# Performance work log

Hardware: AMD Instinct MI355X
Metric: run time of the kernel (lower is better)

The kernel has to match this reference:

```python
import jax, jax.numpy as jnp
import numpy as np

N = 50000          # num nodes
E = 800000         # num edges
NEG_SLOPE = 0.2    # leaky relu slope for attention logits


def gat_layer(h, W, al, ar, src, dst, res_W=None, res_identity=False, apply_elu=False):
    """One GATConv layer (DGL semantics, dropout=0, fc bias-free).
    h: [N, F_in]; W: [F_in, H*D]; al, ar: [H, D]. Returns [N, H, D]."""
    H, D = al.shape
    feat = (h @ W).reshape(N, H, D)                      # projected features
    el = jnp.sum(feat * al, axis=-1)                     # [N, H]
    er = jnp.sum(feat * ar, axis=-1)                     # [N, H]
    e = jax.nn.leaky_relu(el[src] + er[dst], NEG_SLOPE)  # [E, H] edge logits
    # numerically-stable edge softmax segmented over destination nodes
    m = jax.ops.segment_max(e, dst, num_segments=N)      # [N, H]
    m = jnp.where(jnp.isfinite(m), m, 0.0)               # nodes with no in-edges
    ex = jnp.exp(e - m[dst])
    den = jax.ops.segment_sum(ex, dst, num_segments=N)   # [N, H]
    alpha = ex / (den[dst] + 1e-9)                       # [E, H]
    # message passing: gather src feats, weight by alpha, scatter-add to dst
    out = jax.ops.segment_sum(feat[src] * alpha[..., None], dst, num_segments=N)
    if res_identity:
        out = out + h.reshape(N, H, D)
    elif res_W is not None:
        out = out + (h @ res_W).reshape(N, H, D)
    if apply_elu:
        out = jax.nn.elu(out)
    return out


def setup_inputs() -> dict:
    key = jax.random.key(0)
    ks = jax.random.split(key, 14)
    s = 0.1  # keep attention logits tame
    return {
        "features": jax.random.normal(ks[0], (N, 128), jnp.float32),
        "W0": jax.random.normal(ks[1], (128, 128), jnp.float32) * s,
        "al0": jax.random.normal(ks[2], (4, 32), jnp.float32) * s,
        "ar0": jax.random.normal(ks[3], (4, 32), jnp.float32) * s,
        "W1": jax.random.normal(ks[4], (128, 128), jnp.float32) * s,
        "al1": jax.random.normal(ks[5], (4, 32), jnp.float32) * s,
        "ar1": jax.random.normal(ks[6], (4, 32), jnp.float32) * s,
        "W2": jax.random.normal(ks[7], (128, 40), jnp.float32) * s,
        "al2": jax.random.normal(ks[8], (1, 40), jnp.float32) * s,
        "ar2": jax.random.normal(ks[9], (1, 40), jnp.float32) * s,
        "resW2": jax.random.normal(ks[10], (128, 40), jnp.float32) * s,
        "src": jax.random.randint(ks[11], (E,), 0, N, jnp.int32),
        "dst": jax.random.randint(ks[12], (E,), 0, N, jnp.int32),
    }


def reference(features, W0, al0, ar0, W1, al1, ar1, W2, al2, ar2, resW2, src, dst):
    # hidden layer 0: no residual, elu, flatten heads
    h = gat_layer(features, W0, al0, ar0, src, dst, apply_elu=True).reshape(N, -1)
    # hidden layer 1: residual (identity since in == heads*out), elu, flatten
    h = gat_layer(h, W1, al1, ar1, src, dst, res_identity=True, apply_elu=True).reshape(N, -1)
    # output layer: residual projection, no activation, mean over heads
    logits = gat_layer(h, W2, al2, ar2, src, dst, res_W=resW2).mean(axis=1)
    return logits
```

## Files before the change

kernel.cpp:

```cpp
#include <hip/hip_runtime.h>
#include <hip/hip_fp16.h>

#define NNODES 50000
#define NEDGES 800000
#define NBUCK 196
#define NCHUNK 256
#define CHUNK 3125

typedef _Float16 f16x8 __attribute__((ext_vector_type(8)));
typedef float f32x4 __attribute__((ext_vector_type(4)));


__global__ __launch_bounds__(256) void k_packhist(const int* __restrict__ src,
                                                  const int* __restrict__ dst,
                                                  unsigned* __restrict__ pack,
                                                  int* __restrict__ hist) {
  __shared__ int h[NBUCK];
  int t = threadIdx.x, c = blockIdx.x;
  for (int i = t; i < NBUCK; i += 256) h[i] = 0;
  __syncthreads();
  int beg = c * CHUNK;
  for (int q = t; q < CHUNK; q += 256) {
    int e = beg + q;
    unsigned d = (unsigned)dst[e], sv = (unsigned)src[e];
    pack[e] = (d << 16) | sv;
    atomicAdd(&h[d >> 8], 1);
  }
  __syncthreads();
  for (int i = t; i < NBUCK; i += 256) hist[i * NCHUNK + c] = h[i];
}

__global__ __launch_bounds__(1024) void k_scanall(const int* __restrict__ hist,
                                                  int* __restrict__ off) {
  __shared__ int sb[1024];
  int t = threadIdx.x;
  const int P = (NBUCK * NCHUNK) / 1024;
  int base = t * P;
  int s = 0;
  for (int i = 0; i < P; ++i) s += hist[base + i];
  sb[t] = s;
  __syncthreads();
  for (int o = 1; o < 1024; o <<= 1) {
    int x = (t >= o) ? sb[t - o] : 0;
    __syncthreads();
    sb[t] += x;
    __syncthreads();
  }
  int ex = sb[t] - s;
  for (int i = 0; i < P; ++i) {
    int v = hist[base + i];
    off[base + i] = ex;
    ex += v;
  }
}

__global__ __launch_bounds__(256) void k_partition(const unsigned* __restrict__ pack,
                                                   const int* __restrict__ off,
                                                   unsigned* __restrict__ bucketed) {
  __shared__ int cur[NBUCK];
  int t = threadIdx.x, c = blockIdx.x;
  for (int i = t; i < NBUCK; i += 256) cur[i] = off[i * NCHUNK + c];
  __syncthreads();
  int beg = c * CHUNK;
  for (int q = t; q < CHUNK; q += 256) {
    unsigned v = pack[beg + q];
    int pos = atomicAdd(&cur[v >> 24], 1);
    bucketed[pos] = v;
  }
}

__global__ __launch_bounds__(256) void k_sortbkt(const unsigned* __restrict__ bucketed,
                                                 const int* __restrict__ off,
                                                 int* __restrict__ row_off,
                                                 int* __restrict__ esrc) {
  __shared__ int cnt[256];
  __shared__ int cur[256];
  int t = threadIdx.x, b = blockIdx.x;
  int base = off[b * NCHUNK];
  int endb = (b == NBUCK - 1) ? NEDGES : off[(b + 1) * NCHUNK];
  int ne = endb - base;
  cnt[t] = 0;
  __syncthreads();
  for (int i = t; i < ne; i += 256)
    atomicAdd(&cnt[(bucketed[base + i] >> 16) & 255], 1);
  __syncthreads();
  int orig = cnt[t];
  cur[t] = orig;
  __syncthreads();
  for (int o = 1; o < 256; o <<= 1) {
    int x = (t >= o) ? cur[t - o] : 0;
    __syncthreads();
    cur[t] += x;
    __syncthreads();
  }
  int excl = cur[t] - orig;
  int g = (b << 8) + t;
  if (g <= NNODES) row_off[g] = base + excl;
  cur[t] = excl;
  __syncthreads();
  for (int i = t; i < ne; i += 256) {
    unsigned v = bucketed[base + i];
    int pos = base + atomicAdd(&cur[(v >> 16) & 255], 1);
    esrc[pos] = (int)(v & 0xFFFFu);
  }
}

__global__ __launch_bounds__(128) void k_prep(const float* __restrict__ W0, const float* __restrict__ al0,
                                              const float* __restrict__ ar0,
                                              const float* __restrict__ W1, const float* __restrict__ al1,
                                              const float* __restrict__ ar1,
                                              const float* __restrict__ W2, const float* __restrict__ resW2,
                                              const float* __restrict__ al2, const float* __restrict__ ar2,
                                              _Float16* __restrict__ Wt0, _Float16* __restrict__ Wt1,
                                              _Float16* __restrict__ Wt2) {
  int b = blockIdx.x, k = threadIdx.x;
  if (b < 288) {
    const float* W = (b < 144) ? W0 : W1;
    const float* al = (b < 144) ? al0 : al1;
    const float* ar = (b < 144) ? ar0 : ar1;
    _Float16* Wt = (b < 144) ? Wt0 : Wt1;
    int c = (b < 144) ? b : b - 144;
    float v = 0.f;
    if (c < 128) {
      v = W[k * 128 + c];
    } else if (c < 136) {
      int h = c - 128;
      const float* av = (h < 4) ? al : ar;
      int hh = h & 3;
      float s = 0.f;
      for (int d = 0; d < 32; ++d) s += W[k * 128 + hh * 32 + d] * av[hh * 32 + d];
      v = s;
    }
    Wt[c * 128 + k] = (_Float16)v;
  } else {
    int c = b - 288;
    float v = 0.f;
    if (c < 40) {
      v = W2[k * 40 + c];
    } else if (c < 80) {
      v = resW2[k * 40 + (c - 40)];
    } else if (c == 80) {
      float s = 0.f;
      for (int d = 0; d < 40; ++d) s += W2[k * 40 + d] * al2[d];
      v = s;
    } else if (c == 81) {
      float s = 0.f;
      for (int d = 0; d < 40; ++d) s += W2[k * 40 + d] * ar2[d];
      v = s;
    }
    Wt2[c * 128 + k] = (_Float16)v;
  }
}

template <int NCT, bool L2E>
__global__ __launch_bounds__(512) void k_gemm_mfma(const float* __restrict__ A,
                                                   const _Float16* __restrict__ Wtg,
                                                   __half* __restrict__ C,
                                                   float* __restrict__ resOut,
                                                   float* __restrict__ el,
                                                   float* __restrict__ er, int nrows) {
  __shared__ _Float16 Ah[128 * 136];
  __shared__ _Float16 Wl[NCT * 16 * 136];
  int t = threadIdx.x;
  int r0 = blockIdx.x * 128;

  for (int q = t; q < NCT * 16 * 16; q += 512) {
    int row = q >> 4, k8 = (q & 15) * 8;
    *(f16x8*)(&Wl[row * 136 + k8]) = *(const f16x8*)(Wtg + row * 128 + k8);
  }
  #pragma unroll
  for (int p = 0; p < 8; ++p) {
    int q = p * 512 + t;
    int r = q >> 5, k4 = (q & 31) * 4;
    float4 v = make_float4(0.f, 0.f, 0.f, 0.f);
    if (r0 + r < nrows) v = *(const float4*)(A + (size_t)(r0 + r) * 128 + k4);
    union { _Float16 h[4]; uint2 u; } pk;
    pk.h[0] = (_Float16)v.x; pk.h[1] = (_Float16)v.y;
    pk.h[2] = (_Float16)v.z; pk.h[3] = (_Float16)v.w;
    *(uint2*)(&Ah[r * 136 + k4]) = pk.u;
  }
  __syncthreads();

  int wave = t >> 6, l = t & 63;
  const _Float16* abase = &Ah[(wave * 16 + (l & 15)) * 136 + ((l >> 4) * 8)];
  const _Float16* bbase = &Wl[(l & 15) * 136 + ((l >> 4) * 8)];

  f32x4 acc[NCT] = {};
  #pragma unroll
  for (int ks = 0; ks < 4; ++ks) {
    f16x8 af = *(const f16x8*)(abase + ks * 32);
    #pragma unroll
    for (int nt = 0; nt < NCT; ++nt) {
      f16x8 bf = *(const f16x8*)(bbase + nt * 16 * 136 + ks * 32);
      acc[nt] = __builtin_amdgcn_mfma_f32_16x16x32_f16(af, bf, acc[nt], 0, 0, 0);
    }
  }

  int cc = l & 15;
  int rbase = r0 + wave * 16 + (l >> 4) * 4;
  #pragma unroll
  for (int r = 0; r < 4; ++r) {
    int row = rbase + r;
    if (row >= nrows) continue;
    if (!L2E) {
      #pragma unroll
      for (int nt = 0; nt < 8; ++nt)
        C[(size_t)row * 128 + nt * 16 + cc] = __float2half_rn(acc[nt][r]);
      float v = acc[8][r];
      if (cc < 4) el[row * 4 + cc] = v;
      else if (cc < 8) er[row * 4 + (cc - 4)] = v;
    } else {
      #pragma unroll
      for (int nt = 0; nt < 6; ++nt) {
        int col = nt * 16 + cc;
        float v = acc[nt][r];
        if (col < 40) C[(size_t)row * 40 + col] = __float2half_rn(v);
        else if (col < 80) resOut[(size_t)row * 40 + (col - 40)] = v;
        else if (col == 80) el[row] = v;
        else if (col == 81) er[row] = v;
      }
    }
  }
}

__device__ __forceinline__ void fma8h(float4& a0, float4& a1, float w, const uint4& r) {
  const __half2* hp = (const __half2*)&r;
  float2 f0 = __half22float2(hp[0]);
  float2 f1 = __half22float2(hp[1]);
  float2 f2 = __half22float2(hp[2]);
  float2 f3 = __half22float2(hp[3]);
  a0.x += w * f0.x; a0.y += w * f0.y; a0.z += w * f1.x; a0.w += w * f1.y;
  a1.x += w * f2.x; a1.y += w * f2.y; a1.z += w * f3.x; a1.w += w * f3.y;
}

template <bool RES, bool DOELU>
__global__ __launch_bounds__(256) void k_msg128v4(const __half* __restrict__ feat,
                                                  const float* __restrict__ el,
                                                  const float* __restrict__ er,
                                                  const int* __restrict__ row_off,
                                                  const int* __restrict__ esrc,
                                                  const float* __restrict__ hres,
                                                  float* __restrict__ out, int nnodes) {
  int t = threadIdx.x;
  int n = blockIdx.x * 16 + (t >> 4);
  if (n >= nnodes) return;
  int lane = t & 15;
  int h = lane >> 2;
  int s = row_off[n], e = row_off[n + 1];
  float ern = er[n * 4 + h];
  float4 acc0[4] = {}, acc1[4] = {};
  float den[4] = {0.f, 0.f, 0.f, 0.f};

  for (int c = s; c < e; c += 16) {
    int m = e - c; if (m > 16) m = 16;
    int sjv = 0;
    if (lane < m) sjv = esrc[c + lane];
    int e0 = __shfl(sjv, (lane & 3), 16);
    int e1 = __shfl(sjv, (lane & 3) + 4, 16);
    int e2 = __shfl(sjv, (lane & 3) + 8, 16);
    int e3 = __shfl(sjv, (lane & 3) + 12, 16);
    float sel0 = el[e0 * 4 + h];
    float sel1 = el[e1 * 4 + h];
    float sel2 = el[e2 * 4 + h];
    float sel3 = el[e3 * 4 + h];

#define GAT_SUB(KK, SEL)                                                      \
    {                                                                         \
      int b = KK * 4;                                                         \
      if (b < m) {                                                            \
        int mm = m - b; if (mm > 4) mm = 4;                                   \
        _Pragma("unroll")                                                     \
        for (int j = 0; j < 4; ++j) {                                         \
          if (j < mm) {                                                       \
            float ev = __shfl(SEL, (lane & 12) | j, 16);                      \
            float x = ev + ern;                                               \
            x = fmaxf(x, 0.2f * x);                                           \
            float wgt = __expf(x);                                            \
            int sj = __shfl(sjv, b + j, 16);                                  \
            den[j] += wgt;                                                    \
            uint4 raw = *(const uint4*)(feat + (size_t)sj * 128 + lane * 8);  \
            fma8h(acc0[j], acc1[j], wgt, raw);                                \
          }                                                                   \
        }                                                                     \
      }                                                                       \
    }
    GAT_SUB(0, sel0)
    GAT_SUB(1, sel1)
    GAT_SUB(2, sel2)
    GAT_SUB(3, sel3)
#undef GAT_SUB
  }

  float4 A0, A1;
  A0.x = (acc0[0].x + acc0[1].x) + (acc0[2].x + acc0[3].x);
  A0.y = (acc0[0].y + acc0[1].y) + (acc0[2].y + acc0[3].y);
  A0.z = (acc0[0].z + acc0[1].z) + (acc0[2].z + acc0[3].z);
  A0.w = (acc0[0].w + acc0[1].w) + (acc0[2].w + acc0[3].w);
  A1.x = (acc1[0].x + acc1[1].x) + (acc1[2].x + acc1[3].x);
  A1.y = (acc1[0].y + acc1[1].y) + (acc1[2].y + acc1[3].y);
  A1.z = (acc1[0].z + acc1[1].z) + (acc1[2].z + acc1[3].z);
  A1.w = (acc1[0].w + acc1[1].w) + (acc1[2].w + acc1[3].w);
  float D = (den[0] + den[1]) + (den[2] + den[3]);
  float inv = (e > s) ? 1.f / D : 0.f;
  A0.x *= inv; A0.y *= inv; A0.z *= inv; A0.w *= inv;
  A1.x *= inv; A1.y *= inv; A1.z *= inv; A1.w *= inv;
  if (RES) {
    float4 r0 = *(const float4*)(hres + (size_t)n * 128 + lane * 8);
    float4 r1 = *(const float4*)(hres + (size_t)n * 128 + lane * 8 + 4);
    A0.x += r0.x; A0.y += r0.y; A0.z += r0.z; A0.w += r0.w;
    A1.x += r1.x; A1.y += r1.y; A1.z += r1.z; A1.w += r1.w;
  }
  if (DOELU) {
    A0.x = (A0.x > 0.f) ? A0.x : expm1f(A0.x);
    A0.y = (A0.y > 0.f) ? A0.y : expm1f(A0.y);
    A0.z = (A0.z > 0.f) ? A0.z : expm1f(A0.z);
    A0.w = (A0.w > 0.f) ? A0.w : expm1f(A0.w);
    A1.x = (A1.x > 0.f) ? A1.x : expm1f(A1.x);
    A1.y = (A1.y > 0.f) ? A1.y : expm1f(A1.y);
    A1.z = (A1.z > 0.f) ? A1.z : expm1f(A1.z);
    A1.w = (A1.w > 0.f) ? A1.w : expm1f(A1.w);
  }
  *(float4*)(out + (size_t)n * 128 + lane * 8) = A0;
  *(float4*)(out + (size_t)n * 128 + lane * 8 + 4) = A1;
}

__global__ __launch_bounds__(256) void k_msg40v4(const __half* __restrict__ feat,
                                                 const float* __restrict__ el,
                                                 const float* __restrict__ er,
                                                 const int* __restrict__ row_off,
                                                 const int* __restrict__ esrc,
                                                 const float* __restrict__ res,
                                                 float* __restrict__ out, int nnodes) {
  int t = threadIdx.x;
  int n = blockIdx.x * 16 + (t >> 4);
  if (n >= nnodes) return;
  int lane = t & 15;
  int s = row_off[n], e = row_off[n + 1];
  float ern = er[n];
  float4 acc[2] = {};
  float den[2] = {0.f, 0.f};

  for (int c = s; c < e; c += 16) {
    int m = e - c; if (m > 16) m = 16;
    int sjv = 0;
    if (lane < m) sjv = esrc[c + lane];
    float selv = el[sjv];
    #pragma unroll
    for (int j = 0; j < 16; ++j) {
      if (j < m) {
        float ev = __shfl(selv, j, 16);
        float x = ev + ern;
        x = fmaxf(x, 0.2f * x);
        float wgt = __expf(x);
        int sj = __shfl(sjv, j, 16);
        den[j & 1] += wgt;
        if (lane < 10) {
          uint2 raw = *(const uint2*)(feat + (size_t)sj * 40 + lane * 4);
          const __half2* hp = (const __half2*)&raw;
          float2 f0 = __half22float2(hp[0]);
          float2 f1 = __half22float2(hp[1]);
          acc[j & 1].x += wgt * f0.x;
          acc[j & 1].y += wgt * f0.y;
          acc[j & 1].z += wgt * f1.x;
          acc[j & 1].w += wgt * f1.y;
        }
      }
    }
  }
  float D = den[0] + den[1];
  float inv = (e > s) ? 1.f / D : 0.f;
  if (lane < 10) {
    float4 r = *(const float4*)(res + (size_t)n * 40 + lane * 4);
    float4 A;
    A.x = (acc[0].x + acc[1].x) * inv + r.x;
    A.y = (acc[0].y + acc[1].y) * inv + r.y;
    A.z = (acc[0].z + acc[1].z) * inv + r.z;
    A.w = (acc[0].w + acc[1].w) * inv + r.w;
    *(float4*)(out + (size_t)n * 40 + lane * 4) = A;
  }
}

extern "C" void kernel_launch(void* const* d_in, const int* in_sizes, int n_in,
                              void* d_out, int out_size, void* d_ws, size_t ws_size,
                              hipStream_t stream) {
  const float* features = (const float*)d_in[0];
  const float* W0 = (const float*)d_in[1];
  const float* al0 = (const float*)d_in[2];
  const float* ar0 = (const float*)d_in[3];
  const float* W1 = (const float*)d_in[4];
  const float* al1 = (const float*)d_in[5];
  const float* ar1 = (const float*)d_in[6];
  const float* W2 = (const float*)d_in[7];
  const float* al2 = (const float*)d_in[8];
  const float* ar2 = (const float*)d_in[9];
  const float* resW2 = (const float*)d_in[10];
  const int* src = (const int*)d_in[11];
  const int* dst = (const int*)d_in[12];
  float* out = (float*)d_out;

  const int N = NNODES;
  char* w = (char*)d_ws;
  auto alloc = [&](size_t bytes) {
    char* p = w;
    w += (bytes + 255) & ~(size_t)255;
    return p;
  };
  int* row_off = (int*)alloc((size_t)(N + 1) * 4);
  int* esrc = (int*)alloc((size_t)NEDGES * 4);
  unsigned* pack = (unsigned*)alloc((size_t)NEDGES * 4);
  unsigned* bucketed = (unsigned*)alloc((size_t)NEDGES * 4);
  int* hist = (int*)alloc(NBUCK * NCHUNK * 4);
  int* off = (int*)alloc(NBUCK * NCHUNK * 4);
  __half* feath = (__half*)alloc((size_t)N * 128 * 2);
  float* res2 = (float*)alloc((size_t)N * 40 * 4);
  float* el = (float*)alloc((size_t)N * 4 * 4);
  float* er = (float*)alloc((size_t)N * 4 * 4);
  float* h1 = (float*)alloc((size_t)N * 128 * 4);
  float* h2 = (float*)alloc((size_t)N * 128 * 4);
  _Float16* Wt0 = (_Float16*)alloc(144 * 128 * 2);
  _Float16* Wt1 = (_Float16*)alloc(144 * 128 * 2);
  _Float16* Wt2 = (_Float16*)alloc(96 * 128 * 2);
  __half* feat2h = feath;

  k_prep<<<384, 128, 0, stream>>>(W0, al0, ar0, W1, al1, ar1, W2, resW2, al2, ar2,
                                  Wt0, Wt1, Wt2);

  k_packhist<<<NCHUNK, 256, 0, stream>>>(src, dst, pack, hist);
  k_scanall<<<1, 1024, 0, stream>>>(hist, off);
  k_partition<<<NCHUNK, 256, 0, stream>>>(pack, off, bucketed);
  k_sortbkt<<<NBUCK, 256, 0, stream>>>(bucketed, off, row_off, esrc);

  const int GB128 = (N + 127) / 128;
  const int GM = (N + 15) / 16;

  k_gemm_mfma<9, false><<<GB128, 512, 0, stream>>>(features, Wt0, feath, nullptr, el, er, N);
  k_msg128v4<false, true><<<GM, 256, 0, stream>>>(feath, el, er, row_off, esrc, nullptr, h1, N);

  k_gemm_mfma<9, false><<<GB128, 512, 0, stream>>>(h1, Wt1, feath, nullptr, el, er, N);
  k_msg128v4<true, true><<<GM, 256, 0, stream>>>(feath, el, er, row_off, esrc, h1, h2, N);

  k_gemm_mfma<6, true><<<GB128, 512, 0, stream>>>(h2, Wt2, feat2h, res2, el, er, N);
  k_msg40v4<<<GM, 256, 0, stream>>>(feat2h, el, er, row_off, esrc, res2, out, N);
}
```

Before: 202.8 us.

## Store hidden activations in fp16 and compute edge weights once per lane

Hidden layer outputs h1/h2 are now stored as fp16 instead of fp32. The GEMM gets an fp16 input path, and the residual reads fp16 directly, which halves the activation write and read traffic between layers. The message kernels now compute each edge's leaky-relu/exp weight once per lane and broadcast it by shuffle, rather than recomputing it in every lane. The per-edge denominator is reduced with xor shuffles at the end. The risk is extra fp16 rounding on the hidden activations and residuals.

```diff
diff --git a/kernel.cpp b/kernel.cpp
--- a/kernel.cpp
+++ b/kernel.cpp
@@ -152,8 +152,8 @@
   }
 }
 
-template <int NCT, bool L2E>
-__global__ __launch_bounds__(512) void k_gemm_mfma(const float* __restrict__ A,
+template <int NCT, bool L2E, bool AF32>
+__global__ __launch_bounds__(512) void k_gemm_mfma(const void* __restrict__ Av,
                                                    const _Float16* __restrict__ Wtg,
                                                    __half* __restrict__ C,
                                                    float* __restrict__ resOut,
@@ -168,16 +168,30 @@
     int row = q >> 4, k8 = (q & 15) * 8;
     *(f16x8*)(&Wl[row * 136 + k8]) = *(const f16x8*)(Wtg + row * 128 + k8);
   }
-  #pragma unroll
-  for (int p = 0; p < 8; ++p) {
-    int q = p * 512 + t;
-    int r = q >> 5, k4 = (q & 31) * 4;
-    float4 v = make_float4(0.f, 0.f, 0.f, 0.f);
-    if (r0 + r < nrows) v = *(const float4*)(A + (size_t)(r0 + r) * 128 + k4);
-    union { _Float16 h[4]; uint2 u; } pk;
-    pk.h[0] = (_Float16)v.x; pk.h[1] = (_Float16)v.y;
-    pk.h[2] = (_Float16)v.z; pk.h[3] = (_Float16)v.w;
-    *(uint2*)(&Ah[r * 136 + k4]) = pk.u;
+  if (AF32) {
+    const float* A = (const float*)Av;
+    #pragma unroll
+    for (int p = 0; p < 8; ++p) {
+      int q = p * 512 + t;
+      int r = q >> 5, k4 = (q & 31) * 4;
+      float4 v = make_float4(0.f, 0.f, 0.f, 0.f);
+      if (r0 + r < nrows) v = *(const float4*)(A + (size_t)(r0 + r) * 128 + k4);
+      union { _Float16 h[4]; uint2 u; } pk;
+      pk.h[0] = (_Float16)v.x; pk.h[1] = (_Float16)v.y;
+      pk.h[2] = (_Float16)v.z; pk.h[3] = (_Float16)v.w;
+      *(uint2*)(&Ah[r * 136 + k4]) = pk.u;
+    }
+  } else {
+    const __half* A = (const __half*)Av;
+    #pragma unroll
+    for (int p = 0; p < 4; ++p) {
+      int q = p * 512 + t;
+      int r = q >> 4, k8 = (q & 15) * 8;
+      union { f16x8 v; uint4 u; } pk;
+      pk.u = make_uint4(0, 0, 0, 0);
+      if (r0 + r < nrows) pk.v = *(const f16x8*)(A + (size_t)(r0 + r) * 128 + k8);
+      *(f16x8*)(&Ah[r * 136 + k8]) = pk.v;
+    }
   }
   __syncthreads();
 
@@ -224,23 +238,25 @@
 }
 
 __device__ __forceinline__ void fma8h(float4& a0, float4& a1, float w, const uint4& r) {
-  const __half2* hp = (const __half2*)&r;
-  float2 f0 = __half22float2(hp[0]);
-  float2 f1 = __half22float2(hp[1]);
-  float2 f2 = __half22float2(hp[2]);
-  float2 f3 = __half22float2(hp[3]);
-  a0.x += w * f0.x; a0.y += w * f0.y; a0.z += w * f1.x; a0.w += w * f1.y;
-  a1.x += w * f2.x; a1.y += w * f2.y; a1.z += w * f3.x; a1.w += w * f3.y;
+  const __half* hp = (const __half*)&r;
+  a0.x += w * __half2float(hp[0]);
+  a0.y += w * __half2float(hp[1]);
+  a0.z += w * __half2float(hp[2]);
+  a0.w += w * __half2float(hp[3]);
+  a1.x += w * __half2float(hp[4]);
+  a1.y += w * __half2float(hp[5]);
+  a1.z += w * __half2float(hp[6]);
+  a1.w += w * __half2float(hp[7]);
 }
 
 template <bool RES, bool DOELU>
-__global__ __launch_bounds__(256) void k_msg128v4(const __half* __restrict__ feat,
+__global__ __launch_bounds__(256) void k_msg128v5(const __half* __restrict__ feat,
                                                   const float* __restrict__ el,
                                                   const float* __restrict__ er,
                                                   const int* __restrict__ row_off,
                                                   const int* __restrict__ esrc,
-                                                  const float* __restrict__ hres,
-                                                  float* __restrict__ out, int nnodes) {
+                                                  const __half* __restrict__ hres,
+                                                  __half* __restrict__ out, int nnodes) {
   int t = threadIdx.x;
   int n = blockIdx.x * 16 + (t >> 4);
   if (n >= nnodes) return;
@@ -249,47 +265,48 @@
   int s = row_off[n], e = row_off[n + 1];
   float ern = er[n * 4 + h];
   float4 acc0[4] = {}, acc1[4] = {};
-  float den[4] = {0.f, 0.f, 0.f, 0.f};
+  float dpart = 0.f;
+  int hb = h << 2;
 
   for (int c = s; c < e; c += 16) {
     int m = e - c; if (m > 16) m = 16;
-    int sjv = 0;
-    if (lane < m) sjv = esrc[c + lane];
-    int e0 = __shfl(sjv, (lane & 3), 16);
-    int e1 = __shfl(sjv, (lane & 3) + 4, 16);
-    int e2 = __shfl(sjv, (lane & 3) + 8, 16);
-    int e3 = __shfl(sjv, (lane & 3) + 12, 16);
-    float sel0 = el[e0 * 4 + h];
-    float sel1 = el[e1 * 4 + h];
-    float sel2 = el[e2 * 4 + h];
-    float sel3 = el[e3 * 4 + h];
-
-#define GAT_SUB(KK, SEL)                                                      \
-    {                                                                         \
-      int b = KK * 4;                                                         \
-      if (b < m) {                                                            \
-        int mm = m - b; if (mm > 4) mm = 4;                                   \
-        _Pragma("unroll")                                                     \
-        for (int j = 0; j < 4; ++j) {                                         \
-          if (j < mm) {                                                       \
-            float ev = __shfl(SEL, (lane & 12) | j, 16);                      \
-            float x = ev + ern;                                               \
-            x = fmaxf(x, 0.2f * x);                                           \
-            float wgt = __expf(x);                                            \
-            int sj = __shfl(sjv, b + j, 16);                                  \
-            den[j] += wgt;                                                    \
-            uint4 raw = *(const uint4*)(feat + (size_t)sj * 128 + lane * 8);  \
-            fma8h(acc0[j], acc1[j], wgt, raw);                                \
-          }                                                                   \
-        }                                                                     \
-      }                                                                       \
-    }
-    GAT_SUB(0, sel0)
-    GAT_SUB(1, sel1)
-    GAT_SUB(2, sel2)
-    GAT_SUB(3, sel3)
-#undef GAT_SUB
-  }
+    int sjl = (lane < m) ? esrc[c + lane] : 0;
+    int b0 = lane & 3;
+    int e0 = __shfl(sjl, b0, 16);
+    int e1 = __shfl(sjl, b0 + 4, 16);
+    int e2 = __shfl(sjl, b0 + 8, 16);
+    int e3 = __shfl(sjl, b0 + 12, 16);
+    float x0 = el[e0 * 4 + h] + ern;
+    float x1 = el[e1 * 4 + h] + ern;
+    float x2 = el[e2 * 4 + h] + ern;
+    float x3 = el[e3 * 4 + h] + ern;
+    x0 = fmaxf(x0, 0.2f * x0);
+    x1 = fmaxf(x1, 0.2f * x1);
+    x2 = fmaxf(x2, 0.2f * x2);
+    x3 = fmaxf(x3, 0.2f * x3);
+    float w0 = (b0 < m) ? __expf(x0) : 0.f;
+    float w1 = (b0 + 4 < m) ? __expf(x1) : 0.f;
+    float w2 = (b0 + 8 < m) ? __expf(x2) : 0.f;
+    float w3 = (b0 + 12 < m) ? __expf(x3) : 0.f;
+    dpart += (w0 + w1) + (w2 + w3);
+
+#define GAT_J(J, WK)                                                          \
+    if (J < m) {                                                              \
+      float wgt = __shfl(WK, hb | (J & 3), 16);                               \
+      int sj = __shfl(sjl, J, 16);                                            \
+      uint4 raw = *(const uint4*)(feat + (size_t)sj * 128 + lane * 8);        \
+      fma8h(acc0[J & 3], acc1[J & 3], wgt, raw);                              \
+    }
+    GAT_J(0, w0) GAT_J(1, w0) GAT_J(2, w0) GAT_J(3, w0)
+    GAT_J(4, w1) GAT_J(5, w1) GAT_J(6, w1) GAT_J(7, w1)
+    GAT_J(8, w2) GAT_J(9, w2) GAT_J(10, w2) GAT_J(11, w2)
+    GAT_J(12, w3) GAT_J(13, w3) GAT_J(14, w3) GAT_J(15, w3)
+#undef GAT_J
+  }
+
+  float den = dpart;
+  den += __shfl_xor(den, 1, 16);
+  den += __shfl_xor(den, 2, 16);
 
   float4 A0, A1;
   A0.x = (acc0[0].x + acc0[1].x) + (acc0[2].x + acc0[3].x);
@@ -300,15 +317,16 @@
   A1.y = (acc1[0].y + acc1[1].y) + (acc1[2].y + acc1[3].y);
   A1.z = (acc1[0].z + acc1[1].z) + (acc1[2].z + acc1[3].z);
   A1.w = (acc1[0].w + acc1[1].w) + (acc1[2].w + acc1[3].w);
-  float D = (den[0] + den[1]) + (den[2] + den[3]);
-  float inv = (e > s) ? 1.f / D : 0.f;
+  float inv = (e > s) ? 1.f / den : 0.f;
   A0.x *= inv; A0.y *= inv; A0.z *= inv; A0.w *= inv;
   A1.x *= inv; A1.y *= inv; A1.z *= inv; A1.w *= inv;
   if (RES) {
-    float4 r0 = *(const float4*)(hres + (size_t)n * 128 + lane * 8);
-    float4 r1 = *(const float4*)(hres + (size_t)n * 128 + lane * 8 + 4);
-    A0.x += r0.x; A0.y += r0.y; A0.z += r0.z; A0.w += r0.w;
-    A1.x += r1.x; A1.y += r1.y; A1.z += r1.z; A1.w += r1.w;
+    uint4 rr = *(const uint4*)(hres + (size_t)n * 128 + lane * 8);
+    const __half* hp = (const __half*)&rr;
+    A0.x += __half2float(hp[0]); A0.y += __half2float(hp[1]);
+    A0.z += __half2float(hp[2]); A0.w += __half2float(hp[3]);
+    A1.x += __half2float(hp[4]); A1.y += __half2float(hp[5]);
+    A1.z += __half2float(hp[6]); A1.w += __half2float(hp[7]);
   }
   if (DOELU) {
     A0.x = (A0.x > 0.f) ? A0.x : expm1f(A0.x);
@@ -320,11 +338,15 @@
     A1.z = (A1.z > 0.f) ? A1.z : expm1f(A1.z);
     A1.w = (A1.w > 0.f) ? A1.w : expm1f(A1.w);
   }
-  *(float4*)(out + (size_t)n * 128 + lane * 8) = A0;
-  *(float4*)(out + (size_t)n * 128 + lane * 8 + 4) = A1;
-}
-
-__global__ __launch_bounds__(256) void k_msg40v4(const __half* __restrict__ feat,
+  union { __half hh[8]; uint4 u; } pk;
+  pk.hh[0] = __float2half_rn(A0.x); pk.hh[1] = __float2half_rn(A0.y);
+  pk.hh[2] = __float2half_rn(A0.z); pk.hh[3] = __float2half_rn(A0.w);
+  pk.hh[4] = __float2half_rn(A1.x); pk.hh[5] = __float2half_rn(A1.y);
+  pk.hh[6] = __float2half_rn(A1.z); pk.hh[7] = __float2half_rn(A1.w);
+  *(uint4*)(out + (size_t)n * 128 + lane * 8) = pk.u;
+}
+
+__global__ __launch_bounds__(256) void k_msg40v5(const __half* __restrict__ feat,
                                                  const float* __restrict__ el,
                                                  const float* __restrict__ er,
                                                  const int* __restrict__ row_off,
@@ -338,22 +360,20 @@
   int s = row_off[n], e = row_off[n + 1];
   float ern = er[n];
   float4 acc[2] = {};
-  float den[2] = {0.f, 0.f};
+  float dpart = 0.f;
 
   for (int c = s; c < e; c += 16) {
     int m = e - c; if (m > 16) m = 16;
-    int sjv = 0;
-    if (lane < m) sjv = esrc[c + lane];
-    float selv = el[sjv];
+    int sjl = (lane < m) ? esrc[c + lane] : 0;
+    float x = el[sjl] + ern;
+    x = fmaxf(x, 0.2f * x);
+    float wl = (lane < m) ? __expf(x) : 0.f;
+    dpart += wl;
     #pragma unroll
     for (int j = 0; j < 16; ++j) {
       if (j < m) {
-        float ev = __shfl(selv, j, 16);
-        float x = ev + ern;
-        x = fmaxf(x, 0.2f * x);
-        float wgt = __expf(x);
-        int sj = __shfl(sjv, j, 16);
-        den[j & 1] += wgt;
+        float wgt = __shfl(wl, j, 16);
+        int sj = __shfl(sjl, j, 16);
         if (lane < 10) {
           uint2 raw = *(const uint2*)(feat + (size_t)sj * 40 + lane * 4);
           const __half2* hp = (const __half2*)&raw;
@@ -367,8 +387,12 @@
       }
     }
   }
-  float D = den[0] + den[1];
-  float inv = (e > s) ? 1.f / D : 0.f;
+  float den = dpart;
+  den += __shfl_xor(den, 1, 16);
+  den += __shfl_xor(den, 2, 16);
+  den += __shfl_xor(den, 4, 16);
+  den += __shfl_xor(den, 8, 16);
+  float inv = (e > s) ? 1.f / den : 0.f;
   if (lane < 10) {
     float4 r = *(const float4*)(res + (size_t)n * 40 + lane * 4);
     float4 A;
@@ -415,8 +439,8 @@
   float* res2 = (float*)alloc((size_t)N * 40 * 4);
   float* el = (float*)alloc((size_t)N * 4 * 4);
   float* er = (float*)alloc((size_t)N * 4 * 4);
-  float* h1 = (float*)alloc((size_t)N * 128 * 4);
-  float* h2 = (float*)alloc((size_t)N * 128 * 4);
+  __half* h1 = (__half*)alloc((size_t)N * 128 * 2);
+  __half* h2 = (__half*)alloc((size_t)N * 128 * 2);
   _Float16* Wt0 = (_Float16*)alloc(144 * 128 * 2);
   _Float16* Wt1 = (_Float16*)alloc(144 * 128 * 2);
   _Float16* Wt2 = (_Float16*)alloc(96 * 128 * 2);
@@ -433,12 +457,12 @@
   const int GB128 = (N + 127) / 128;
   const int GM = (N + 15) / 16;
 
-  k_gemm_mfma<9, false><<<GB128, 512, 0, stream>>>(features, Wt0, feath, nullptr, el, er, N);
-  k_msg128v4<false, true><<<GM, 256, 0, stream>>>(feath, el, er, row_off, esrc, nullptr, h1, N);
-
-  k_gemm_mfma<9, false><<<GB128, 512, 0, stream>>>(h1, Wt1, feath, nullptr, el, er, N);
-  k_msg128v4<true, true><<<GM, 256, 0, stream>>>(feath, el, er, row_off, esrc, h1, h2, N);
-
-  k_gemm_mfma<6, true><<<GB128, 512, 0, stream>>>(h2, Wt2, feat2h, res2, el, er, N);
-  k_msg40v4<<<GM, 256, 0, stream>>>(feat2h, el, er, row_off, esrc, res2, out, N);
-}
+  k_gemm_mfma<9, false, true><<<GB128, 512, 0, stream>>>(features, Wt0, feath, nullptr, el, er, N);
+  k_msg128v5<false, true><<<GM, 256, 0, stream>>>(feath, el, er, row_off, esrc, nullptr, h1, N);
+
+  k_gemm_mfma<9, false, false><<<GB128, 512, 0, stream>>>(h1, Wt1, feath, nullptr, el, er, N);
+  k_msg128v5<true, true><<<GM, 256, 0, stream>>>(feath, el, er, row_off, esrc, h1, h2, N);
+
+  k_gemm_mfma<6, true, false><<<GB128, 512, 0, stream>>>(h2, Wt2, feat2h, res2, el, er, N);
+  k_msg40v5<<<GM, 256, 0, stream>>>(feat2h, el, er, row_off, esrc, res2, out, N);
+}
```

After: 203.7 us, median of 2. No clear change (+0.4%).
